# Performance work log

Hardware: AMD Instinct MI355X
Metric: run time of the kernel (lower is better)

## Reference

```python
import jax, jax.numpy as jnp
import numpy as np

B, N, H, W, C = 4, 200000, 512, 512, 64
P, R = 150000, 100000
STAT_THRES = 0.5


def _lin(key, fan_in, fan_out):
    kw, kb = jax.random.split(key)
    s = 1.0 / np.sqrt(fan_in)
    return (jax.random.uniform(kw, (fan_in, fan_out), jnp.float32, -s, s),
            jax.random.uniform(kb, (fan_out,), jnp.float32, -s, s))


def setup_inputs() -> dict:
    key = jax.random.key(0)
    ks = jax.random.split(key, 16)
    W_flow, b_flow = _lin(ks[8], 70, 32)
    W_pc, b_pc = _lin(ks[9], 96, 32)
    W1, b1 = _lin(ks[10], 64, 32)
    W2, b2 = _lin(ks[11], 32, 16)
    W3, b3 = _lin(ks[12], 16, 1)
    return {
        "pc0_map": jax.random.normal(ks[0], (B, C, H, W), jnp.float32),
        "flow_map": jax.random.normal(ks[1], (B, C, H, W), jnp.float32),
        "pc0_fea": jax.random.normal(ks[2], (B, N, 32), jnp.float32),
        "flows": jax.random.normal(ks[3], (B, N, 3), jnp.float32),
        "pose_flows": jax.random.normal(ks[4], (B, P, 3), jnp.float32),
        "radar_pose_flows": jax.random.normal(ks[5], (B, R, 3), jnp.float32),
        "voxel_coords": jax.random.randint(ks[6], (B, N, 3), 0, H),
        "point_idxes": jax.random.randint(ks[7], (B, N), 0, P + R),
        "W_flow": W_flow, "b_flow": b_flow,
        "W_pc": W_pc, "b_pc": b_pc,
        "W1": W1, "b1": b1, "W2": W2, "b2": b2, "W3": W3, "b3": b3,
    }


def reference(pc0_map, flow_map, pc0_fea, flows, pose_flows, radar_pose_flows,
              voxel_coords, point_idxes,
              W_flow, b_flow, W_pc, b_pc, W1, b1, W2, b2, W3, b3):
    vy = voxel_coords[..., 1]  # [B, N]
    vx = voxel_coords[..., 2]  # [B, N]
    # gather per-pillar vectors from dense CHW maps (as HWC for contiguous gather)
    gather = jax.vmap(lambda m, y, x: m[y, x])  # m: [H, W, C]
    pc0_vec = gather(jnp.transpose(pc0_map, (0, 2, 3, 1)), vy, vx)    # [B, N, 64]
    flow_vec = gather(jnp.transpose(flow_map, (0, 2, 3, 1)), vy, vx)  # [B, N, 64]
    # pose_flow = concat(pose, radar_pose)[point_idxes]
    pose_full = jnp.concatenate([pose_flows, radar_pose_flows], axis=1)  # [B, P+R, 3]
    pose = jnp.take_along_axis(pose_full, point_idxes[..., None], axis=1)  # [B, N, 3]
    concat_flow = jnp.concatenate([flow_vec, flows, pose], axis=-1)  # [B, N, 70]
    concat_pc = jnp.concatenate([pc0_vec, pc0_fea], axis=-1)         # [B, N, 96]
    flow_feat = concat_flow @ W_flow + b_flow  # [B, N, 32]
    pc_feat = concat_pc @ W_pc + b_pc          # [B, N, 32]
    h = jnp.concatenate([flow_feat, pc_feat], axis=-1)  # [B, N, 64]
    h = jax.nn.gelu(h @ W1 + b1, approximate=False)
    h = jax.nn.gelu(h @ W2 + b2, approximate=False)
    score = jax.nn.sigmoid((h @ W3 + b3)[..., 0])  # [B, N]
    mask = score > STAT_THRES
    return (mask, score)
```

## Files before the change

### kernel.cpp

```cpp
#include <hip/hip_runtime.h>

#define NB 4
#define NN 200000
#define HH 512
#define WW 512
#define CC 64
#define PP 150000
#define RP 100000
#define HWSZ (HH * WW)
#define NPTS (NB * NN)
#define NPIX (NB * HWSZ)

#define WB_WCAT 0
#define WB_WTAIL 5120
#define WB_BCAT 5312
#define WB_BFRAG 5376
#define WB_BFRAG2 (WB_BFRAG + 3072)
#define WBUF_WORDS (WB_BFRAG2 + 256)

typedef _Float16 half8_t __attribute__((ext_vector_type(8)));
typedef _Float16 half2_t __attribute__((ext_vector_type(2)));
typedef float f32x4 __attribute__((ext_vector_type(4)));

__device__ __forceinline__ unsigned packh(float a, float b) {
    half2_t h; h.x = (_Float16)a; h.y = (_Float16)b;
    unsigned u; __builtin_memcpy(&u, &h, 4); return u;
}
__device__ __forceinline__ float gelu(float v) {
    return 0.5f * v * (1.0f + erff(v * 0.70710678118654752f));
}


__global__ __launch_bounds__(256) void prep1(
    const float* __restrict__ Wf, const float* __restrict__ bf,
    const float* __restrict__ Wp, const float* __restrict__ bp,
    const float* __restrict__ W1, const float* __restrict__ b1,
    float* __restrict__ wbuf)
{
    int g = blockIdx.x * 256 + threadIdx.x;

    if (g < 5120) {
        int r = g >> 5, j = g & 31;
        float s = 0.f;
        if (r < 64) {
            for (int k = 0; k < 32; ++k) s += Wf[r * 32 + k] * W1[k * 32 + j];
        } else {
            int rr = r - 64;
            for (int k = 0; k < 32; ++k) s += Wp[rr * 32 + k] * W1[(32 + k) * 32 + j];
        }
        wbuf[WB_WCAT + g] = s;
    } else if (g < 5312) {
        int idx = g - 5120;
        int r = idx >> 5, j = idx & 31;
        float s = 0.f;
        for (int k = 0; k < 32; ++k) s += Wf[(64 + r) * 32 + k] * W1[k * 32 + j];
        wbuf[WB_WTAIL + idx] = s;
    } else if (g < 5344) {
        int j = g - 5312;
        float s = b1[j];
        for (int k = 0; k < 32; ++k)
            s += bf[k] * W1[k * 32 + j] + bp[k] * W1[(32 + k) * 32 + j];
        wbuf[WB_BCAT + j] = s;
    }
}


__device__ __forceinline__ float wrowf(const float* __restrict__ wbuf, int k, int col) {
    if (k < 160) return wbuf[WB_WCAT + k * 32 + col];
    if (k < 166) return wbuf[WB_WTAIL + (k - 160) * 32 + col];
    if (k == 166) return wbuf[WB_BCAT + col];
    return 0.f;
}

__global__ __launch_bounds__(1024) void prep2(
    const float* __restrict__ wbufc, float* __restrict__ wbuf,
    const float* __restrict__ W2)
{
    int t = threadIdx.x;
    unsigned* BF = (unsigned*)(wbuf + WB_BFRAG);
    for (int idx = t; idx < 3072 + 256; idx += 1024) {
        if (idx < 3072) {
            int w = idx & 3;
            int slot = idx >> 2;
            int l = slot & 63;
            int rest = slot >> 6;
            int tt = rest % 6, nt = rest / 6;
            int k = tt * 32 + (l >> 4) * 8 + w * 2;
            int col = nt * 16 + (l & 15);
            BF[idx] = packh(wrowf(wbufc, k, col), wrowf(wbufc, k + 1, col));
        } else {
            int i2 = idx - 3072;
            int w = i2 & 3, l = i2 >> 2;
            int k2 = (l >> 4) * 8 + w * 2, col = l & 15;
            BF[i2 + 3072] = packh(W2[k2 * 16 + col], W2[(k2 + 1) * 16 + col]);
        }
    }
}


__global__ __launch_bounds__(256) void conv_map(
    const float* __restrict__ pc0_map, const float* __restrict__ flow_map,
    const float* __restrict__ wbuf, _Float16* __restrict__ zmap)
{
    __shared__ uint4 Bf[832];
    __shared__ __align__(16) _Float16 zl[4][16 * 48];
    {
        const uint4* wsrc = (const uint4*)(wbuf + WB_BFRAG);
        for (int i = threadIdx.x; i < 832; i += 256) Bf[i] = wsrc[i];
    }
    __syncthreads();

    int wv = threadIdx.x >> 6;
    int lane = threadIdx.x & 63;
    int lo = lane & 15, hi = lane >> 4;
    size_t p = (size_t)blockIdx.x * 64 + wv * 16 + lo;
    int b = (int)(p >> 18);
    size_t inb = p & (size_t)(HWSZ - 1);

    const float* fm = flow_map + (size_t)b * CC * HWSZ + inb;
    const float* pm = pc0_map  + (size_t)b * CC * HWSZ + inb;

    half8_t A[4];
    #pragma unroll
    for (int t = 0; t < 4; ++t) {
        const float* mp = (t < 2) ? fm : pm;
        int ch0 = (t & 1) * 32 + hi * 8;
        float v[8];
        #pragma unroll
        for (int j = 0; j < 8; ++j) v[j] = mp[(size_t)(ch0 + j) * HWSZ];
        #pragma unroll
        for (int j = 0; j < 8; ++j) A[t][j] = (_Float16)v[j];
    }

    f32x4 acc0 = {0.f, 0.f, 0.f, 0.f};
    f32x4 acc1 = {0.f, 0.f, 0.f, 0.f};
    #pragma unroll
    for (int t = 0; t < 4; ++t) {
        half8_t B0, B1;
        uint4 u0 = Bf[t * 64 + lane];
        uint4 u1 = Bf[(6 + t) * 64 + lane];
        __builtin_memcpy(&B0, &u0, 16);
        __builtin_memcpy(&B1, &u1, 16);
        acc0 = __builtin_amdgcn_mfma_f32_16x16x32_f16(A[t], B0, acc0, 0, 0, 0);
        acc1 = __builtin_amdgcn_mfma_f32_16x16x32_f16(A[t], B1, acc1, 0, 0, 0);
    }

    _Float16* zw = zl[wv];
    #pragma unroll
    for (int r = 0; r < 4; ++r) {
        zw[(hi * 4 + r) * 48 + lo]      = (_Float16)acc0[r];
        zw[(hi * 4 + r) * 48 + 16 + lo] = (_Float16)acc1[r];
    }
    size_t plo = (size_t)blockIdx.x * 64 + wv * 16 + lo;
    uint4 ov;
    __builtin_memcpy(&ov, &zw[lo * 48 + hi * 8], 16);
    *(uint4*)&zmap[plo * 32 + hi * 8] = ov;
}


__global__ __launch_bounds__(512, 8) void point_mlp(
    const _Float16* __restrict__ zmap,
    const float* __restrict__ pc0_fea, const float* __restrict__ flows,
    const float* __restrict__ pose_flows, const float* __restrict__ radar_pose,
    const int* __restrict__ point_idxes, const int* __restrict__ voxel,
    const float* __restrict__ wbuf,
    const float* __restrict__ b2, const float* __restrict__ W3,
    const float* __restrict__ b3,
    float* __restrict__ out)
{
    __shared__ uint4 Bf[832];
    __shared__ __align__(16) _Float16 zl[8][16 * 48];
    {
        const uint4* wsrc = (const uint4*)(wbuf + WB_BFRAG);
        for (int i = threadIdx.x; i < 832; i += 512) Bf[i] = wsrc[i];
    }
    __syncthreads();

    int wv = threadIdx.x >> 6;
    int lane = threadIdx.x & 63;
    int lo = lane & 15, hi = lane >> 4;
    int pid0 = (blockIdx.x * 8 + wv) * 16;
    int pid = pid0 + lo;
    int b = pid0 / NN;

    half8_t A4;
    {
        const f32x4* fe4 = (const f32x4*)(pc0_fea + (size_t)pid * 32 + hi * 8);
        f32x4 fa = fe4[0];
        f32x4 fb = fe4[1];
        A4[0] = (_Float16)fa.x; A4[1] = (_Float16)fa.y;
        A4[2] = (_Float16)fa.z; A4[3] = (_Float16)fa.w;
        A4[4] = (_Float16)fb.x; A4[5] = (_Float16)fb.y;
        A4[6] = (_Float16)fb.z; A4[7] = (_Float16)fb.w;
    }
    half8_t A5;
    {
        #pragma unroll
        for (int j = 0; j < 8; ++j) A5[j] = (_Float16)0.f;
        if (hi == 0) {
            const float* fl = flows + (size_t)pid * 3;
            int pi = point_idxes[pid];
            const float* ps = (pi < PP) ? (pose_flows + ((size_t)b * PP + pi) * 3)
                                        : (radar_pose + ((size_t)b * RP + (pi - PP)) * 3);
            A5[0] = (_Float16)fl[0]; A5[1] = (_Float16)fl[1]; A5[2] = (_Float16)fl[2];
            A5[3] = (_Float16)ps[0]; A5[4] = (_Float16)ps[1]; A5[5] = (_Float16)ps[2];
            A5[6] = (_Float16)1.0f;
        }
    }
    half8_t A6;
    {
        int y = voxel[(size_t)pid * 3 + 1];
        int x = voxel[(size_t)pid * 3 + 2];
        size_t pix = ((size_t)b << 18) + (size_t)y * WW + x;
        uint4 zr = *(const uint4*)&zmap[pix * 32 + hi * 8];
        __builtin_memcpy(&A6, &zr, 16);
    }
    half8_t B60, B61;
    {
        unsigned w0[4], w1[4];
        #pragma unroll
        for (int w = 0; w < 4; ++w) {
            int k0 = hi * 8 + 2 * w, k1 = k0 + 1;
            unsigned a = 0, bmask = 0;
            if (k0 == lo) a |= 0x3C00u;
            if (k1 == lo) a |= 0x3C000000u;
            if (k0 == lo + 16) bmask |= 0x3C00u;
            if (k1 == lo + 16) bmask |= 0x3C000000u;
            w0[w] = a; w1[w] = bmask;
        }
        __builtin_memcpy(&B60, w0, 16);
        __builtin_memcpy(&B61, w1, 16);
    }

    f32x4 acc0 = {0.f, 0.f, 0.f, 0.f};
    f32x4 acc1 = {0.f, 0.f, 0.f, 0.f};
    acc0 = __builtin_amdgcn_mfma_f32_16x16x32_f16(A6, B60, acc0, 0, 0, 0);
    acc1 = __builtin_amdgcn_mfma_f32_16x16x32_f16(A6, B61, acc1, 0, 0, 0);
    {
        half8_t B0, B1;
        uint4 u0 = Bf[4 * 64 + lane];
        uint4 u1 = Bf[(6 + 4) * 64 + lane];
        __builtin_memcpy(&B0, &u0, 16);
        __builtin_memcpy(&B1, &u1, 16);
        acc0 = __builtin_amdgcn_mfma_f32_16x16x32_f16(A4, B0, acc0, 0, 0, 0);
        acc1 = __builtin_amdgcn_mfma_f32_16x16x32_f16(A4, B1, acc1, 0, 0, 0);
        uint4 u2 = Bf[5 * 64 + lane];
        uint4 u3 = Bf[(6 + 5) * 64 + lane];
        __builtin_memcpy(&B0, &u2, 16);
        __builtin_memcpy(&B1, &u3, 16);
        acc0 = __builtin_amdgcn_mfma_f32_16x16x32_f16(A5, B0, acc0, 0, 0, 0);
        acc1 = __builtin_amdgcn_mfma_f32_16x16x32_f16(A5, B1, acc1, 0, 0, 0);
    }

    _Float16* zw = zl[wv];
    #pragma unroll
    for (int r = 0; r < 4; ++r) {
        zw[(hi * 4 + r) * 48 + lo]      = (_Float16)gelu(acc0[r]);
        zw[(hi * 4 + r) * 48 + 16 + lo] = (_Float16)gelu(acc1[r]);
    }

    half8_t A2, B2;
    __builtin_memcpy(&A2, &zw[lo * 48 + hi * 8], 16);
    {
        uint4 u2 = Bf[768 + lane];
        __builtin_memcpy(&B2, &u2, 16);
    }
    f32x4 zz4 = {0.f, 0.f, 0.f, 0.f};
    f32x4 acc2 = __builtin_amdgcn_mfma_f32_16x16x32_f16(A2, B2, zz4, 0, 0, 0);

    float b2v = b2[lo];
    float w3v = W3[lo];
    float e0 = gelu(acc2[0] + b2v) * w3v;
    float e1 = gelu(acc2[1] + b2v) * w3v;
    float e2 = gelu(acc2[2] + b2v) * w3v;
    float e3 = gelu(acc2[3] + b2v) * w3v;
    #pragma unroll
    for (int m = 1; m <= 8; m <<= 1) {
        e0 += __shfl_xor(e0, m);
        e1 += __shfl_xor(e1, m);
        e2 += __shfl_xor(e2, m);
        e3 += __shfl_xor(e3, m);
    }
    int p2 = hi * 4 + lo;
    if (lo < 4) {
        float zs = (lo == 0 ? e0 : lo == 1 ? e1 : lo == 2 ? e2 : e3) + b3[0];
        float score = 1.0f / (1.0f + expf(-zs));
        int pid2 = pid0 + p2;
        out[(size_t)NPTS + pid2] = score;
        out[pid2] = (score > 0.5f) ? 1.0f : 0.0f;
    }
}

extern "C" void kernel_launch(void* const* d_in, const int* in_sizes, int n_in,
                              void* d_out, int out_size, void* d_ws, size_t ws_size,
                              hipStream_t stream) {
    const float* pc0_map    = (const float*)d_in[0];
    const float* flow_map   = (const float*)d_in[1];
    const float* pc0_fea    = (const float*)d_in[2];
    const float* flows      = (const float*)d_in[3];
    const float* pose_flows = (const float*)d_in[4];
    const float* radar_pose = (const float*)d_in[5];
    const int*   voxel      = (const int*)d_in[6];
    const int*   pidx       = (const int*)d_in[7];
    const float* W_flow = (const float*)d_in[8];
    const float* b_flow = (const float*)d_in[9];
    const float* W_pc   = (const float*)d_in[10];
    const float* b_pc   = (const float*)d_in[11];
    const float* W1     = (const float*)d_in[12];
    const float* b1     = (const float*)d_in[13];
    const float* W2     = (const float*)d_in[14];
    const float* b2     = (const float*)d_in[15];
    const float* W3     = (const float*)d_in[16];
    const float* b3     = (const float*)d_in[17];

    size_t need = (size_t)WBUF_WORDS * sizeof(float)
                + (size_t)NPIX * 32 * sizeof(_Float16);
    if (ws_size < need) return;
    float* wbuf = (float*)d_ws;
    _Float16* zmap = (_Float16*)(wbuf + WBUF_WORDS);

    hipLaunchKernelGGL(prep1, dim3(21), dim3(256), 0, stream,
                       W_flow, b_flow, W_pc, b_pc, W1, b1, wbuf);
    hipLaunchKernelGGL(prep2, dim3(1), dim3(1024), 0, stream, wbuf, wbuf, W2);
    hipLaunchKernelGGL(conv_map, dim3(NPIX / 64), dim3(256), 0, stream,
                       pc0_map, flow_map, wbuf, zmap);
    hipLaunchKernelGGL(point_mlp, dim3(NPTS / 128), dim3(512), 0, stream,
                       zmap, pc0_fea, flows, pose_flows, radar_pose,
                       pidx, voxel, wbuf, b2, W3, b3, (float*)d_out);
}
```

Before: 194.3 us.

## Stage map tiles through swizzled LDS with vector loads and register prefetch

conv_map now handles 256 pixels per block. Each wave issues 16-byte loads of 32 contiguous channel rows into a swizzled LDS tile, where the old code read scalar floats at a large channel stride. The next 32-channel tile is prefetched into registers while MFMAs consume the current one. This targets poor coalescing on the dominant read of the two dense maps, at the cost of about 32KB more LDS per block, which lowers occupancy, and extra barriers.

```diff
diff --git a/kernel.cpp b/kernel.cpp
--- a/kernel.cpp
+++ b/kernel.cpp
@@ -10,6 +10,8 @@
 #define HWSZ (HH * WW)
 #define NPTS (NB * NN)
 #define NPIX (NB * HWSZ)
+#define PIXB 256
+#define ROWDW 256
 
 #define WB_WCAT 0
 #define WB_WTAIL 5120
@@ -103,58 +105,89 @@
     const float* __restrict__ wbuf, _Float16* __restrict__ zmap)
 {
     __shared__ uint4 Bf[832];
+    __shared__ __align__(16) float pts32[32 * ROWDW];
     __shared__ __align__(16) _Float16 zl[4][16 * 48];
+
     {
         const uint4* wsrc = (const uint4*)(wbuf + WB_BFRAG);
         for (int i = threadIdx.x; i < 832; i += 256) Bf[i] = wsrc[i];
     }
-    __syncthreads();
-
-    int wv = threadIdx.x >> 6;
-    int lane = threadIdx.x & 63;
+
+    int tid = threadIdx.x;
+    int lane = tid & 63, wv = tid >> 6;
     int lo = lane & 15, hi = lane >> 4;
-    size_t p = (size_t)blockIdx.x * 64 + wv * 16 + lo;
-    int b = (int)(p >> 18);
-    size_t inb = p & (size_t)(HWSZ - 1);
-
-    const float* fm = flow_map + (size_t)b * CC * HWSZ + inb;
-    const float* pm = pc0_map  + (size_t)b * CC * HWSZ + inb;
-
-    half8_t A[4];
+    size_t pixbase = (size_t)blockIdx.x * PIXB;
+    int b = (int)(pixbase >> 18);
+    size_t inb = pixbase & (size_t)(HWSZ - 1);
+
+    const float* fmb = flow_map + (size_t)b * CC * HWSZ + inb;
+    const float* pmb = pc0_map  + (size_t)b * CC * HWSZ + inb;
+
+    f32x4 ld[8];
+    {
+        const float* base = fmb + (size_t)(wv * 8) * HWSZ + 4 * lane;
+        #pragma unroll
+        for (int i = 0; i < 8; ++i)
+            ld[i] = *(const f32x4*)(base + (size_t)i * HWSZ);
+    }
+
+    f32x4 acc0[4], acc1[4];
     #pragma unroll
+    for (int r = 0; r < 4; ++r) {
+        acc0[r] = (f32x4){0.f, 0.f, 0.f, 0.f};
+        acc1[r] = (f32x4){0.f, 0.f, 0.f, 0.f};
+    }
+
     for (int t = 0; t < 4; ++t) {
-        const float* mp = (t < 2) ? fm : pm;
-        int ch0 = (t & 1) * 32 + hi * 8;
-        float v[8];
-        #pragma unroll
-        for (int j = 0; j < 8; ++j) v[j] = mp[(size_t)(ch0 + j) * HWSZ];
-        #pragma unroll
-        for (int j = 0; j < 8; ++j) A[t][j] = (_Float16)v[j];
-    }
-
-    f32x4 acc0 = {0.f, 0.f, 0.f, 0.f};
-    f32x4 acc1 = {0.f, 0.f, 0.f, 0.f};
-    #pragma unroll
-    for (int t = 0; t < 4; ++t) {
+        __syncthreads();
+        #pragma unroll
+        for (int i = 0; i < 8; ++i) {
+            int ch = wv * 8 + i;
+            unsigned addr = ((unsigned)(ch * ROWDW + 4 * lane)) * 4u;
+            addr ^= ((unsigned)(ch >> 3) & 3u) << 5;
+            *(f32x4*)((char*)pts32 + addr) = ld[i];
+        }
+        __syncthreads();
+        if (t < 3) {
+            int tn = t + 1;
+            const float* mb = (tn < 2) ? fmb : pmb;
+            const float* base = mb + (size_t)((tn & 1) * 32 + wv * 8) * HWSZ + 4 * lane;
+            #pragma unroll
+            for (int i = 0; i < 8; ++i)
+                ld[i] = *(const f32x4*)(base + (size_t)i * HWSZ);
+        }
         half8_t B0, B1;
-        uint4 u0 = Bf[t * 64 + lane];
-        uint4 u1 = Bf[(6 + t) * 64 + lane];
-        __builtin_memcpy(&B0, &u0, 16);
-        __builtin_memcpy(&B1, &u1, 16);
-        acc0 = __builtin_amdgcn_mfma_f32_16x16x32_f16(A[t], B0, acc0, 0, 0, 0);
-        acc1 = __builtin_amdgcn_mfma_f32_16x16x32_f16(A[t], B1, acc1, 0, 0, 0);
+        __builtin_memcpy(&B0, &Bf[t * 64 + lane], 16);
+        __builtin_memcpy(&B1, &Bf[(6 + t) * 64 + lane], 16);
+        #pragma unroll
+        for (int tt = 0; tt < 4; ++tt) {
+            int px = wv * 64 + tt * 16 + lo;
+            half8_t A;
+            #pragma unroll
+            for (int j = 0; j < 8; ++j) {
+                int ch = hi * 8 + j;
+                unsigned addr = ((unsigned)(ch * ROWDW + px)) * 4u;
+                addr ^= ((unsigned)(ch >> 3) & 3u) << 5;
+                A[j] = (_Float16)(*(const float*)((const char*)pts32 + addr));
+            }
+            acc0[tt] = __builtin_amdgcn_mfma_f32_16x16x32_f16(A, B0, acc0[tt], 0, 0, 0);
+            acc1[tt] = __builtin_amdgcn_mfma_f32_16x16x32_f16(A, B1, acc1[tt], 0, 0, 0);
+        }
     }
 
     _Float16* zw = zl[wv];
     #pragma unroll
-    for (int r = 0; r < 4; ++r) {
-        zw[(hi * 4 + r) * 48 + lo]      = (_Float16)acc0[r];
-        zw[(hi * 4 + r) * 48 + 16 + lo] = (_Float16)acc1[r];
-    }
-    size_t plo = (size_t)blockIdx.x * 64 + wv * 16 + lo;
-    uint4 ov;
-    __builtin_memcpy(&ov, &zw[lo * 48 + hi * 8], 16);
-    *(uint4*)&zmap[plo * 32 + hi * 8] = ov;
+    for (int tt = 0; tt < 4; ++tt) {
+        #pragma unroll
+        for (int r = 0; r < 4; ++r) {
+            zw[(hi * 4 + r) * 48 + lo]      = (_Float16)acc0[tt][r];
+            zw[(hi * 4 + r) * 48 + 16 + lo] = (_Float16)acc1[tt][r];
+        }
+        size_t pg = pixbase + wv * 64 + tt * 16 + lo;
+        uint4 ov;
+        __builtin_memcpy(&ov, &zw[lo * 48 + hi * 8], 16);
+        *(uint4*)&zmap[pg * 32 + hi * 8] = ov;
+    }
 }
 
 
@@ -322,7 +355,7 @@
     hipLaunchKernelGGL(prep1, dim3(21), dim3(256), 0, stream,
                        W_flow, b_flow, W_pc, b_pc, W1, b1, wbuf);
     hipLaunchKernelGGL(prep2, dim3(1), dim3(1024), 0, stream, wbuf, wbuf, W2);
-    hipLaunchKernelGGL(conv_map, dim3(NPIX / 64), dim3(256), 0, stream,
+    hipLaunchKernelGGL(conv_map, dim3(NPIX / PIXB), dim3(256), 0, stream,
                        pc0_map, flow_map, wbuf, zmap);
     hipLaunchKernelGGL(point_mlp, dim3(NPTS / 128), dim3(512), 0, stream,
                        zmap, pc0_fea, flows, pose_flows, radar_pose,
```

After: 186.0 us. 1.04x faster.
